# Performance work log

Measured on AMD Instinct MI355X. Metric: run time of the kernel, lower is better.

The kernel has to match this reference:

```python
import jax, jax.numpy as jnp
import numpy as np

N = 50000
E_RAND = 800000
F_IN = 256
F_OUT = 256
ALPHA = 0.2  # LeakyReLU negative slope


def setup_inputs() -> dict:
    key = jax.random.key(0)
    k1, k2, k3, k4 = jax.random.split(key, 4)
    x = jax.random.normal(k1, (N, F_IN), dtype=jnp.float32)
    # random edges + self-loops so every row has at least one edge (avoids div by 0)
    edge_rand = jax.random.randint(k2, (2, E_RAND), 0, N)
    loops = jnp.arange(N)
    edge = jnp.concatenate([edge_rand, jnp.stack([loops, loops])], axis=1)  # [2, 850000]
    W = jax.random.normal(k3, (F_IN, F_OUT), dtype=jnp.float32) * 0.05
    a = jax.random.normal(k4, (2 * F_OUT,), dtype=jnp.float32) * 0.05
    return {"x": x, "edge": edge, "W": W, "a": a}


def reference(x, edge, W, a):
    # x: [N, F_in], edge: [2, E] (row = dst/aggregation index per torch.sparse.mm(a, h))
    n = x.shape[0]
    f_out = W.shape[1]
    h = x @ W  # [N, F_out]
    src, dst = edge[0], edge[1]
    # a @ [h_src; h_dst] decomposes into two per-node dot products (no [E, 2F] concat)
    s = h @ a[:f_out]   # [N]
    t = h @ a[f_out:]   # [N]
    logit = s[src] + t[dst]                                  # [E]
    e = jnp.exp(-jax.nn.leaky_relu(logit, ALPHA))            # [E]
    rowsum = jax.ops.segment_sum(e, src, num_segments=n)     # [N]
    msg = e[:, None] * h[dst]                                # [E, F_out]
    h_prime = jax.ops.segment_sum(msg, src, num_segments=n)  # [N, F_out]
    h_prime = h_prime / rowsum[:, None]
    return jax.nn.relu(h_prime)  # concat=True path
```

## Files before the change

kernel.cpp:

```cpp
#include <hip/hip_runtime.h>
#include <hip/hip_fp16.h>

#define FDIM 256
#define ALPHA 0.2f

typedef _Float16 half8 __attribute__((ext_vector_type(8)));
typedef float floatx4 __attribute__((ext_vector_type(4)));

__global__ __launch_bounds__(256) void prep_hist(const float* __restrict__ W,
                                                 _Float16* __restrict__ wswz,
                                                 const int* __restrict__ edge,
                                                 int* __restrict__ deg, int E) {
  if (blockIdx.x < 32) {
    const int g = blockIdx.x * 256 + threadIdx.x;
    const int kc = g >> 11, L = g & 2047;
    const int n = L >> 3, c = L & 7;
    half8 hv;
#pragma unroll
    for (int j = 0; j < 8; ++j)
      hv[j] = (_Float16)W[(size_t)(kc * 64 + c * 8 + j) * 256 + n];
    *(half8*)(wswz + (size_t)g * 8) = hv;
  } else {
    const int e = (blockIdx.x - 32) * 256 + threadIdx.x;
    if (e < E) atomicAdd(&deg[edge[e]], 1);
  }
}

#define HT_STRIDE 264
__global__ __launch_bounds__(256) void gemm_mfma(
    const float* __restrict__ x, const _Float16* __restrict__ wswz,
    const float* __restrict__ a, _Float16* __restrict__ h,
    float* __restrict__ s, float* __restrict__ t, int M) {
  __shared__ __align__(16) _Float16 smem[64 * HT_STRIDE];
  _Float16* As = smem;
  const int tid = threadIdx.x;
  const int w = tid >> 6, l = tid & 63;
  const int l15 = l & 15, q = l >> 4;
  const int row0 = blockIdx.x * 64;

  floatx4 acc[4][4];
#pragma unroll
  for (int mt = 0; mt < 4; ++mt)
#pragma unroll
    for (int nt = 0; nt < 4; ++nt) acc[mt][nt] = (floatx4){0.f, 0.f, 0.f, 0.f};

#pragma unroll
  for (int kc = 0; kc < 4; ++kc)
#pragma unroll
    for (int hf = 0; hf < 2; ++hf) {
      const int id = hf * 256 + tid;
      const int m = id >> 3;
      const int c = (id & 7) ^ (m & 7);
      const int row = row0 + m;
      float4 f0 = make_float4(0.f, 0.f, 0.f, 0.f);
      float4 f1 = make_float4(0.f, 0.f, 0.f, 0.f);
      if (row < M) {
        const float4* p =
            (const float4*)(x + (size_t)row * 256 + kc * 64 + c * 8);
        f0 = p[0];
        f1 = p[1];
      }
      half8 hv;
      hv[0] = (_Float16)f0.x; hv[1] = (_Float16)f0.y;
      hv[2] = (_Float16)f0.z; hv[3] = (_Float16)f0.w;
      hv[4] = (_Float16)f1.x; hv[5] = (_Float16)f1.y;
      hv[6] = (_Float16)f1.z; hv[7] = (_Float16)f1.w;
      *(half8*)(As + (size_t)(kc * 512 + id) * 8) = hv;
    }
  __syncthreads();

#pragma unroll 2
  for (int ks = 0; ks < 8; ++ks) {
    const int kc = ks >> 1;
    const int c = (ks & 1) * 4 + q;
    half8 bf[4];
#pragma unroll
    for (int nt = 0; nt < 4; ++nt) {
      const int n = w * 64 + nt * 16 + l15;
      bf[nt] = *(const half8*)(wswz + (size_t)(kc * 2048 + n * 8 + c) * 8);
    }
    half8 af[4];
#pragma unroll
    for (int mt = 0; mt < 4; ++mt) {
      const int m = mt * 16 + l15;
      af[mt] =
          *(const half8*)(As + (size_t)(kc * 512 + m * 8 + (c ^ (m & 7))) * 8);
    }
#pragma unroll
    for (int mt = 0; mt < 4; ++mt)
#pragma unroll
      for (int nt = 0; nt < 4; ++nt)
        acc[mt][nt] = __builtin_amdgcn_mfma_f32_16x16x32_f16(
            af[mt], bf[nt], acc[mt][nt], 0, 0, 0);
  }
  __syncthreads();

#pragma unroll
  for (int mt = 0; mt < 4; ++mt)
#pragma unroll
    for (int nt = 0; nt < 4; ++nt)
#pragma unroll
      for (int r = 0; r < 4; ++r)
        smem[(size_t)(mt * 16 + q * 4 + r) * HT_STRIDE + w * 64 + nt * 16 +
             l15] = (_Float16)acc[mt][nt][r];
  __syncthreads();

  const int w8 = tid >> 5;
  const int colh = (tid & 31) * 8;
#pragma unroll
  for (int p = 0; p < 8; ++p) {
    const int rl = p * 8 + w8;
    const int row = row0 + rl;
    if (row < M)
      *(half8*)(h + (size_t)row * 256 + colh) =
          *(const half8*)(smem + (size_t)rl * HT_STRIDE + colh);
  }

  const int r8 = tid >> 2, seg = tid & 3;
  float sp = 0.f, tp = 0.f;
#pragma unroll
  for (int c8 = 0; c8 < 8; ++c8) {
    const int col = seg * 64 + c8 * 8;
    const half8 hv = *(const half8*)(smem + (size_t)r8 * HT_STRIDE + col);
    const float4 a0 = *(const float4*)(a + col);
    const float4 a1 = *(const float4*)(a + col + 4);
    const float4 b0 = *(const float4*)(a + 256 + col);
    const float4 b1 = *(const float4*)(a + 256 + col + 4);
    sp += (float)hv[0] * a0.x + (float)hv[1] * a0.y + (float)hv[2] * a0.z +
          (float)hv[3] * a0.w + (float)hv[4] * a1.x + (float)hv[5] * a1.y +
          (float)hv[6] * a1.z + (float)hv[7] * a1.w;
    tp += (float)hv[0] * b0.x + (float)hv[1] * b0.y + (float)hv[2] * b0.z +
          (float)hv[3] * b0.w + (float)hv[4] * b1.x + (float)hv[5] * b1.y +
          (float)hv[6] * b1.z + (float)hv[7] * b1.w;
  }
  sp += __shfl_xor(sp, 1);
  sp += __shfl_xor(sp, 2);
  tp += __shfl_xor(tp, 1);
  tp += __shfl_xor(tp, 2);
  if (seg == 0 && row0 + r8 < M) {
    s[row0 + r8] = sp;
    t[row0 + r8] = tp;
  }
}

__global__ __launch_bounds__(1024) void scan1(const int* __restrict__ deg,
                                              int* __restrict__ rowstart,
                                              int* __restrict__ bsum, int n) {
  const int tid = threadIdx.x;
  const int i = blockIdx.x * 1024 + tid;
  const int val = (i < n) ? deg[i] : 0;
  const int lane = tid & 63, wv = tid >> 6;
  int v = val;
#pragma unroll
  for (int off = 1; off < 64; off <<= 1) {
    const int o = __shfl_up(v, off);
    if (lane >= off) v += o;
  }
  __shared__ int wsum[16];
  __shared__ int woff[16];
  if (lane == 63) wsum[wv] = v;
  __syncthreads();
  if (tid < 16) {
    int wv2 = wsum[tid];
#pragma unroll
    for (int off = 1; off < 16; off <<= 1) {
      const int o = __shfl_up(wv2, off);
      if (tid >= off) wv2 += o;
    }
    woff[tid] = wv2;
  }
  __syncthreads();
  const int incl = v + (wv ? woff[wv - 1] : 0);
  if (i < n) rowstart[i] = incl - val;
  if (tid == 1023) bsum[blockIdx.x] = woff[15];
}

__global__ __launch_bounds__(1024) void scan3(int* __restrict__ rowstart,
                                              int* __restrict__ rsc,
                                              const int* __restrict__ bsum,
                                              int n, int nb) {
  __shared__ int sboff;
  const int tid = threadIdx.x;
  if (tid < 64) {
    const int v = (tid < nb) ? bsum[tid] : 0;
    int pre = (tid < (int)blockIdx.x) ? v : 0;
    int tot = v;
#pragma unroll
    for (int off = 32; off > 0; off >>= 1) {
      pre += __shfl_xor(pre, off);
      tot += __shfl_xor(tot, off);
    }
    if (tid == 0) {
      sboff = pre;
      if (blockIdx.x == (unsigned)(nb - 1)) rowstart[n] = tot;
    }
  }
  __syncthreads();
  const int i = blockIdx.x * 1024 + tid;
  if (i < n) {
    const int v = rowstart[i] + sboff;
    rowstart[i] = v;
    rsc[i] = v;
  }
}

__global__ void scatter_kernel(const int* __restrict__ edge,
                               int* __restrict__ rsc, int* __restrict__ sdst,
                               int E) {
  const int e = blockIdx.x * 256 + threadIdx.x;
  if (e < E) {
    const int src = edge[e];
    const int dst = edge[E + e];
    const int pos = atomicAdd(&rsc[src], 1);
    sdst[pos] = dst;
  }
}

__global__ __launch_bounds__(256) void agg_kernel(
    const _Float16* __restrict__ h, const float* __restrict__ s,
    const float* __restrict__ t, const int* __restrict__ rowstart,
    const int* __restrict__ sdst, float* __restrict__ out, int n) {
  const int w = threadIdx.x >> 6, l = threadIdx.x & 63;
  const int row = blockIdx.x * 4 + w;
  if (row >= n) return;
  const int start = rowstart[row], end = rowstart[row + 1];
  const float srow = s[row];
  const int half = l >> 5;
  const int lh = l & 31;
  const size_t fo = (size_t)lh * 8;
  float acc[8] = {};
  float rs = 0.f;
  int j = start;
  for (; j + 8 <= end; j += 8) {
#pragma unroll
    for (int u = 0; u < 4; ++u) {
      const int d = sdst[j + u * 2 + half];
      const float logit = srow + t[d];
      const float lr = logit > 0.f ? logit : ALPHA * logit;
      const float e = __expf(-lr);
      const half8 v = *(const half8*)(h + (size_t)d * 256 + fo);
      rs += e;
#pragma unroll
      for (int k = 0; k < 8; ++k) acc[k] += e * (float)v[k];
    }
  }
  for (; j < end; j += 2) {
    const int idx = j + half;
    const bool valid = idx < end;
    const int d = valid ? sdst[idx] : 0;
    const float logit = srow + t[d];
    const float lr = logit > 0.f ? logit : ALPHA * logit;
    const float e = valid ? __expf(-lr) : 0.f;
    const half8 v = *(const half8*)(h + (size_t)d * 256 + fo);
    rs += e;
#pragma unroll
    for (int k = 0; k < 8; ++k) acc[k] += e * (float)v[k];
  }
  rs += __shfl_xor(rs, 32);
#pragma unroll
  for (int k = 0; k < 8; ++k) acc[k] += __shfl_xor(acc[k], 32);
  const float inv = 1.f / rs;
  float4 o;
#pragma unroll
  for (int k = 0; k < 4; ++k) {
    const float vv = acc[half * 4 + k] * inv;
    (&o.x)[k] = vv > 0.f ? vv : 0.f;
  }
  *(float4*)(out + (size_t)row * 256 + lh * 8 + half * 4) = o;
}

extern "C" void kernel_launch(void* const* d_in, const int* in_sizes, int n_in,
                              void* d_out, int out_size, void* d_ws,
                              size_t ws_size, hipStream_t stream) {
  const float* x = (const float*)d_in[0];
  const int* edge = (const int*)d_in[1];
  const float* W = (const float*)d_in[2];
  const float* a = (const float*)d_in[3];
  float* out = (float*)d_out;
  const int N = in_sizes[0] / FDIM;
  const int E = in_sizes[1] / 2;
  const int NB = (N + 1023) / 1024;

  _Float16* h = (_Float16*)d_ws;
  _Float16* wswz = h + (size_t)N * FDIM;
  float* s = (float*)(wswz + 8192 * 8);
  float* t = s + N;
  int* deg = (int*)(t + N);
  int* rsc = deg + N;
  int* rowstart = rsc + N;
  int* bsum = rowstart + N + 2;
  int* sdst = bsum + 64;

  hipMemsetAsync(deg, 0, (size_t)N * sizeof(int), stream);

  prep_hist<<<32 + (E + 255) / 256, 256, 0, stream>>>(W, wswz, edge, deg, E);
  gemm_mfma<<<(N + 63) / 64, 256, 0, stream>>>(x, wswz, a, h, s, t, N);
  scan1<<<NB, 1024, 0, stream>>>(deg, rowstart, bsum, N);
  scan3<<<NB, 1024, 0, stream>>>(rowstart, rsc, bsum, N, NB);
  scatter_kernel<<<(E + 255) / 256, 256, 0, stream>>>(edge, rsc, sdst, E);
  agg_kernel<<<(N + 3) / 4, 256, 0, stream>>>(h, s, t, rowstart, sdst, out, N);
}
```

Measured before the change: 287.8 us.

## Fuse edge scatter into GEMM launch and batch four edges per thread

Moves the CSR scatter into the GEMM kernel as extra leading blocks, so the scatter (atomic-bound) and the MFMA GEMM run concurrently in one launch. The GEMM now runs after the scans instead of before them. The histogram and scatter loops also process four edges per thread to raise memory-level parallelism. The cost is that scatter blocks reserve the GEMM's shared-memory footprint and that their placement competes with GEMM blocks.

```diff
diff --git a/kernel.cpp b/kernel.cpp
--- a/kernel.cpp
+++ b/kernel.cpp
@@ -21,22 +21,56 @@
       hv[j] = (_Float16)W[(size_t)(kc * 64 + c * 8 + j) * 256 + n];
     *(half8*)(wswz + (size_t)g * 8) = hv;
   } else {
-    const int e = (blockIdx.x - 32) * 256 + threadIdx.x;
-    if (e < E) atomicAdd(&deg[edge[e]], 1);
+    const int base = (blockIdx.x - 32) * 1024 + threadIdx.x;
+    int srcs[4];
+#pragma unroll
+    for (int u = 0; u < 4; ++u) {
+      const int e = base + u * 256;
+      srcs[u] = (e < E) ? edge[e] : -1;
+    }
+#pragma unroll
+    for (int u = 0; u < 4; ++u)
+      if (srcs[u] >= 0) atomicAdd(&deg[srcs[u]], 1);
   }
 }
 
 #define HT_STRIDE 264
-__global__ __launch_bounds__(256) void gemm_mfma(
+__global__ __launch_bounds__(256) void gemm_scatter(
     const float* __restrict__ x, const _Float16* __restrict__ wswz,
     const float* __restrict__ a, _Float16* __restrict__ h,
-    float* __restrict__ s, float* __restrict__ t, int M) {
+    float* __restrict__ s, float* __restrict__ t, int M,
+    const int* __restrict__ edge, int* __restrict__ rsc,
+    int* __restrict__ sdst, int E, int SB) {
   __shared__ __align__(16) _Float16 smem[64 * HT_STRIDE];
+  const int tid = threadIdx.x;
+
+  if ((int)blockIdx.x < SB) {
+    const int base = blockIdx.x * 1024 + tid;
+    int srcs[4], dsts[4];
+#pragma unroll
+    for (int u = 0; u < 4; ++u) {
+      const int e = base + u * 256;
+      if (e < E) {
+        srcs[u] = edge[e];
+        dsts[u] = edge[E + e];
+      } else {
+        srcs[u] = -1;
+      }
+    }
+    int pos[4];
+#pragma unroll
+    for (int u = 0; u < 4; ++u)
+      if (srcs[u] >= 0) pos[u] = atomicAdd(&rsc[srcs[u]], 1);
+#pragma unroll
+    for (int u = 0; u < 4; ++u)
+      if (srcs[u] >= 0) sdst[pos[u]] = dsts[u];
+    return;
+  }
+
   _Float16* As = smem;
-  const int tid = threadIdx.x;
   const int w = tid >> 6, l = tid & 63;
   const int l15 = l & 15, q = l >> 4;
-  const int row0 = blockIdx.x * 64;
+  const int row0 = (blockIdx.x - SB) * 64;
 
   floatx4 acc[4][4];
 #pragma unroll
@@ -204,18 +238,6 @@
   }
 }
 
-__global__ void scatter_kernel(const int* __restrict__ edge,
-                               int* __restrict__ rsc, int* __restrict__ sdst,
-                               int E) {
-  const int e = blockIdx.x * 256 + threadIdx.x;
-  if (e < E) {
-    const int src = edge[e];
-    const int dst = edge[E + e];
-    const int pos = atomicAdd(&rsc[src], 1);
-    sdst[pos] = dst;
-  }
-}
-
 __global__ __launch_bounds__(256) void agg_kernel(
     const _Float16* __restrict__ h, const float* __restrict__ s,
     const float* __restrict__ t, const int* __restrict__ rowstart,
@@ -293,10 +315,12 @@
 
   hipMemsetAsync(deg, 0, (size_t)N * sizeof(int), stream);
 
-  prep_hist<<<32 + (E + 255) / 256, 256, 0, stream>>>(W, wswz, edge, deg, E);
-  gemm_mfma<<<(N + 63) / 64, 256, 0, stream>>>(x, wswz, a, h, s, t, N);
+  const int EB = (E + 1023) / 1024;
+  prep_hist<<<32 + EB, 256, 0, stream>>>(W, wswz, edge, deg, E);
   scan1<<<NB, 1024, 0, stream>>>(deg, rowstart, bsum, N);
   scan3<<<NB, 1024, 0, stream>>>(rowstart, rsc, bsum, N, NB);
-  scatter_kernel<<<(E + 255) / 256, 256, 0, stream>>>(edge, rsc, sdst, E);
+  const int GB = (N + 63) / 64;
+  gemm_scatter<<<EB + GB, 256, 0, stream>>>(x, wswz, a, h, s, t, N, edge, rsc,
+                                            sdst, E, EB);
   agg_kernel<<<(N + 3) / 4, 256, 0, stream>>>(h, s, t, rowstart, sdst, out, N);
 }
```

New measurement: 273.7 us. 1.05x faster.
